# Optimization experiments

Measured on AMD Instinct MI355X. Metric: run time of the kernel, lower is better.

## Reference

```python
import jax, jax.numpy as jnp
import numpy as np
import math
from jax import lax

BATCH, SEQ_LEN, ENC_IN = 8, 2048, 1
D_MODEL, N_HEADS, E_LAYERS, D_FF, FACTOR, C_OUT = 512, 8, 3, 512, 5, 2
EPS = 1e-5


def _layernorm(x, g, b):
    mu = x.mean(-1, keepdims=True)
    var = ((x - mu) ** 2).mean(-1, keepdims=True)
    return (x - mu) / jnp.sqrt(var + EPS) * g + b


def _prob_attention(q, k, v, key):
    # q,k,v: [B,H,L,Dh]; ProbSparse: sample U keys per query, pick top-u queries by M = max - mean
    B, H, L, Dh = q.shape
    U = min(FACTOR * int(np.ceil(np.log(L))), L)  # U_part == u since L_Q == L_K
    idx = jax.random.randint(key, (L, U), 0, L)   # sampled key indices per query
    k_samp = k[:, :, idx, :]                       # [B,H,L,U,Dh]
    qk = jnp.einsum('bhld,bhlud->bhlu', q, k_samp)
    M = qk.max(-1) - qk.mean(-1)                   # sparsity measure [B,H,L]
    _, top = lax.top_k(M, U)                       # active query indices [B,H,U]
    q_red = jnp.take_along_axis(q, top[..., None], axis=2)
    scores = jnp.einsum('bhud,bhkd->bhuk', q_red, k) * (1.0 / math.sqrt(Dh))
    A = jax.nn.softmax(scores, axis=-1)
    ctx = jnp.broadcast_to(v.mean(axis=2, keepdims=True), q.shape)  # lazy-query context = mean(V)
    upd = jnp.einsum('bhuk,bhkd->bhud', A, v)
    b = jnp.arange(B)[:, None, None]
    h = jnp.arange(H)[None, :, None]
    return ctx.at[b, h, top].set(upd)


def _encoder_layer(x, p, key):
    Wq, Wk, Wv, bq, bk, bv, Wo, bo, W1, b1, W2, b2, g1, be1, g2, be2 = p
    B, L, dm = x.shape
    Dh = dm // N_HEADS
    split = lambda t: t.reshape(B, L, N_HEADS, Dh).transpose(0, 2, 1, 3)
    q = split(x @ Wq.T + bq)
    k = split(x @ Wk.T + bk)
    v = split(x @ Wv.T + bv)
    o = _prob_attention(q, k, v, key).transpose(0, 2, 1, 3).reshape(B, L, dm)
    x = _layernorm(x + o @ Wo.T + bo, g1, be1)
    y = jax.nn.gelu(x @ W1.T + b1, approximate=False) @ W2.T + b2  # 1x1 convs == linears
    return _layernorm(x + y, g2, be2)


def _distil_conv(x, w, b, g, be):
    # Conv1d(dm,dm,3, circular pad) -> BatchNorm(eval) -> ELU -> MaxPool1d(3, stride 2, pad 1)
    xc = jnp.pad(x.transpose(0, 2, 1), ((0, 0), (0, 0), (1, 1)), mode='wrap')
    y = lax.conv_general_dilated(xc, w, (1,), 'VALID', dimension_numbers=('NCH', 'OIH', 'NCH'))
    y = y + b[None, :, None]
    y = y / np.float32(np.sqrt(1.0 + EPS)) * g[None, :, None] + be[None, :, None]
    y = jax.nn.elu(y)
    y = lax.reduce_window(y, -jnp.inf, lax.max, (1, 1, 3), (1, 1, 2), [(0, 0), (0, 0), (1, 1)])
    return y.transpose(0, 2, 1)


def _forward(x_enc, tok_w, Wq, Wk, Wv, bq, bk, bv, Wo, bo, W1, b1, W2, b2,
             ln1_g, ln1_b, ln2_g, ln2_b, dc_w, dc_b, bn_g, bn_b, lnf_g, lnf_b, proj_w, proj_b):
    B, L = x_enc.shape
    dm = D_MODEL
    # TokenEmbedding: circular Conv1d(1, d_model, 3, bias=False)
    xc = jnp.pad(x_enc[:, None, :], ((0, 0), (0, 0), (1, 1)), mode='wrap')
    tok = lax.conv_general_dilated(xc, tok_w, (1,), 'VALID', dimension_numbers=('NCH', 'OIH', 'NCH'))
    tok = tok.transpose(0, 2, 1)  # [B,L,dm]
    # fixed sinusoidal positional embedding
    pos = jnp.arange(L, dtype=jnp.float32)[:, None]
    div = jnp.exp(jnp.arange(0, dm, 2, dtype=jnp.float32) * (-math.log(10000.0) / dm))
    pe = jnp.zeros((L, dm), jnp.float32).at[:, 0::2].set(jnp.sin(pos * div)).at[:, 1::2].set(jnp.cos(pos * div))
    x = tok + pe[None]
    key = jax.random.key(42)
    for i in range(E_LAYERS):
        p = (Wq[i], Wk[i], Wv[i], bq[i], bk[i], bv[i], Wo[i], bo[i],
             W1[i], b1[i], W2[i], b2[i], ln1_g[i], ln1_b[i], ln2_g[i], ln2_b[i])
        x = _encoder_layer(x, p, jax.random.fold_in(key, i))
        if i < E_LAYERS - 1:
            x = _distil_conv(x, dc_w[i], dc_b[i], bn_g[i], bn_b[i])
    x = _layernorm(x, lnf_g, lnf_b)
    return x.max(axis=1) @ proj_w.T + proj_b  # [B, C_OUT]


def setup_inputs() -> dict:
    key = jax.random.key(0)
    ks = jax.random.split(key, 12)
    dm, dff, L = D_MODEL, D_FF, E_LAYERS
    w = lambda k, shape, fan: jax.random.normal(k, shape, jnp.float32) / np.float32(np.sqrt(fan))
    return {
        'x_enc': jax.random.normal(ks[0], (BATCH, SEQ_LEN), jnp.float32),
        'tok_w': w(ks[1], (dm, ENC_IN, 3), 3 * ENC_IN),
        'Wq': w(ks[2], (L, dm, dm), dm), 'Wk': w(ks[3], (L, dm, dm), dm),
        'Wv': w(ks[4], (L, dm, dm), dm), 'Wo': w(ks[5], (L, dm, dm), dm),
        'bq': jnp.zeros((L, dm)), 'bk': jnp.zeros((L, dm)),
        'bv': jnp.zeros((L, dm)), 'bo': jnp.zeros((L, dm)),
        'W1': w(ks[6], (L, dff, dm), dm), 'b1': jnp.zeros((L, dff)),
        'W2': w(ks[7], (L, dm, dff), dff), 'b2': jnp.zeros((L, dm)),
        'ln1_g': jnp.ones((L, dm)), 'ln1_b': jnp.zeros((L, dm)),
        'ln2_g': jnp.ones((L, dm)), 'ln2_b': jnp.zeros((L, dm)),
        'dc_w': w(ks[8], (L - 1, dm, dm, 3), 3 * dm), 'dc_b': jnp.zeros((L - 1, dm)),
        'bn_g': jnp.ones((L - 1, dm)), 'bn_b': jnp.zeros((L - 1, dm)),
        'lnf_g': jnp.ones((dm,)), 'lnf_b': jnp.zeros((dm,)),
        'proj_w': w(ks[9], (C_OUT, dm), dm), 'proj_b': jnp.zeros((C_OUT,)),
    }


def reference(x_enc, tok_w, Wq, Wk, Wv, bq, bk, bv, Wo, bo, W1, b1, W2, b2,
              ln1_g, ln1_b, ln2_g, ln2_b, dc_w, dc_b, bn_g, bn_b, lnf_g, lnf_b, proj_w, proj_b):
    return _forward(x_enc, tok_w, Wq, Wk, Wv, bq, bk, bv, Wo, bo, W1, b1, W2, b2,
                    ln1_g, ln1_b, ln2_g, ln2_b, dc_w, dc_b, bn_g, bn_b, lnf_g, lnf_b, proj_w, proj_b)
```

## Files before the change

### kernel.cpp

```cpp
#include <hip/hip_runtime.h>

#define B_ 8
#define H_ 8
#define DM 512
#define DH 64
#define LMAX 2048
#define COUT 2

typedef __attribute__((ext_vector_type(8))) short frag8;
typedef __attribute__((ext_vector_type(4))) float f32x4;

typedef __attribute__((address_space(1))) const unsigned int guint;
typedef __attribute__((address_space(3))) unsigned int luint;
__device__ __forceinline__ void dma16(const short* g, short* l) {
  __builtin_amdgcn_global_load_lds((guint*)g, (luint*)l, 16, 0, 0);
}

__device__ __forceinline__ short f2bf(float v) {
  unsigned u = __float_as_uint(v);
  unsigned r = (u + 0x7fffu + ((u >> 16) & 1u)) >> 16;
  return (short)r;
}
__device__ __forceinline__ float bf2f(short s) {
  return __uint_as_float(((unsigned)(unsigned short)s) << 16);
}

__device__ __forceinline__ void tf2x32(unsigned k0, unsigned k1, unsigned x0, unsigned x1,
                                       unsigned& o0, unsigned& o1) {
  unsigned ks2 = k0 ^ k1 ^ 0x1BD11BDAu;
  x0 += k0; x1 += k1;
#define RND(r) { x0 += x1; x1 = (x1 << r) | (x1 >> (32 - r)); x1 ^= x0; }
  RND(13) RND(15) RND(26) RND(6)  x0 += k1;  x1 += ks2 + 1u;
  RND(17) RND(29) RND(16) RND(24) x0 += ks2; x1 += k0 + 2u;
  RND(13) RND(15) RND(26) RND(6)  x0 += k0;  x1 += k1 + 3u;
  RND(17) RND(29) RND(16) RND(24) x0 += k1;  x1 += ks2 + 4u;
  RND(13) RND(15) RND(26) RND(6)  x0 += ks2; x1 += k0 + 5u;
#undef RND
  o0 = x0; o1 = x1;
}

__global__ void idx_kernel(int* __restrict__ idxArr, int L, int U, int layer) {
  int p = blockIdx.x * 256 + threadIdx.x;
  int half = L * U;
  if (p >= half) return;
  unsigned fk0, fk1, k20, k21, o0, o1;
  tf2x32(0u, 42u, 0u, (unsigned)layer, fk0, fk1);
  tf2x32(fk0, fk1, 0u, 1u, k20, k21);
  tf2x32(k20, k21, 0u, (unsigned)p, o0, o1);
  idxArr[p] = (int)((o0 ^ o1) & (unsigned)(L - 1));
}

__global__ void embed_kernel(const float* __restrict__ xe, const float* __restrict__ tw,
                             float* __restrict__ X) {
  int i = blockIdx.x * 256 + threadIdx.x;
  int c = i % DM;
  int l = (i / DM) % LMAX;
  int b = i / (DM * LMAX);
  int lm = (l + LMAX - 1) & (LMAX - 1);
  int lp = (l + 1) & (LMAX - 1);
  const float* xb = xe + b * LMAX;
  float tok = tw[c * 3 + 0] * xb[lm] + tw[c * 3 + 1] * xb[l] + tw[c * 3 + 2] * xb[lp];
  float freq = expf(-(float)(c & ~1) * (9.210340371976184f / 512.0f));
  float ang = (float)l * freq;
  float pe = (c & 1) ? cosf(ang) : sinf(ang);
  X[i] = tok + pe;
}

__global__ void wsplit_kernel(const float* __restrict__ W, short* __restrict__ P0,
                              short* __restrict__ P1, short* __restrict__ P2, int n) {
  int i = blockIdx.x * 256 + threadIdx.x;
  if (i >= n) return;
  float v = W[i];
  short h0 = f2bf(v);
  float r1 = v - bf2f(h0);
  short h1 = f2bf(r1);
  float r2 = r1 - bf2f(h1);
  P0[i] = h0; P1[i] = h1; P2[i] = f2bf(r2);
}

__global__ void wt3_kernel(const float* __restrict__ w, short* __restrict__ P0,
                           short* __restrict__ P1, short* __restrict__ P2) {
  int i = blockIdx.x * 256 + threadIdx.x;
  int n = i / 1536, r = i - n * 1536, tap = r >> 9, k = r & 511;
  float v = w[((size_t)n * DM + k) * 3 + tap];
  short h0 = f2bf(v);
  float r1 = v - bf2f(h0);
  short h1 = f2bf(r1);
  float r2 = r1 - bf2f(h1);
  P0[i] = h0; P1[i] = h1; P2[i] = f2bf(r2);
}

template <int ACT, int QKV, int ACC, int CONV>
__global__ __launch_bounds__(256) void mgemm(const short* __restrict__ A0g,
                                             const short* __restrict__ A1g,
                                             const short* __restrict__ A2g,
                                             const short* __restrict__ W0g,
                                             const short* __restrict__ W1g,
                                             const short* __restrict__ W2g,
                                             const float* __restrict__ bias,
                                             float* __restrict__ C, int L, int Ktot) {
  __shared__ short A0[128 * 32], A1[128 * 32], A2[128 * 32];
  __shared__ short B0[128 * 32], B1[128 * 32], B2[128 * 32];
  int tid = threadIdx.x;
  int lane = tid & 63, wave = tid >> 6;
  int crow = lane >> 2, ckq = lane & 3;
  int gx = gridDim.x;
  int flat = blockIdx.y * gx + blockIdx.x;
  int mB, nB;
  if ((gridDim.y & 7) == 0) {
    int phase = flat & 7, sup = flat >> 3;
    nB = sup % gx;
    mB = phase + 8 * (sup / gx);
  } else {
    nB = blockIdx.x; mB = blockIdx.y;
  }
  int n0 = nB * 128, m0 = mB * 128;
  int wm = (wave >> 1) * 64, wn = (wave & 1) * 64;
  f32x4 acc[4][4] = {};
  int lrow = lane & 15, lq = lane >> 4;

  for (int k0 = 0; k0 < Ktot; k0 += 32) {
    int tap = 0, kcol = k0;
    if (CONV) { tap = k0 >> 9; kcol = k0 & 511; }
#pragma unroll
    for (int q = 0; q < 6; ++q) {
      int gc = wave * 6 + q;
      int pl = gc >> 3, c = gc & 7;
      int grow = m0 + c * 16 + crow;
      const short* gp;
      if (CONV) {
        int b = grow / L, l = grow - b * L;
        int le = l + tap - 1;
        le = (le < 0) ? le + L : (le >= L ? le - L : le);
        gp = ((size_t)(b * L + le) * DM + kcol + ckq * 8) +
             (pl == 0 ? A0g : pl == 1 ? A1g : A2g);
      } else {
        gp = ((size_t)grow * DM + k0 + ckq * 8) +
             (pl == 0 ? A0g : pl == 1 ? A1g : A2g);
      }
      short* lp = (pl == 0 ? A0 : pl == 1 ? A1 : A2) + c * 512;
      dma16(gp, lp);
    }
#pragma unroll
    for (int q = 0; q < 6; ++q) {
      int gc = wave * 6 + q;
      int pl = gc >> 3, c = gc & 7;
      int grow = n0 + c * 16 + crow;
      const short* gp = ((size_t)grow * Ktot + k0 + ckq * 8) +
                        (pl == 0 ? W0g : pl == 1 ? W1g : W2g);
      short* lp = (pl == 0 ? B0 : pl == 1 ? B1 : B2) + c * 512;
      dma16(gp, lp);
    }
    __syncthreads();
    frag8 a0f[4], a1f[4], a2f[4];
#pragma unroll
    for (int ti = 0; ti < 4; ++ti) {
      int off = (wm + ti * 16 + lrow) * 32 + lq * 8;
      a0f[ti] = *(const frag8*)&A0[off];
      a1f[ti] = *(const frag8*)&A1[off];
      a2f[ti] = *(const frag8*)&A2[off];
    }
#pragma unroll
    for (int tj = 0; tj < 4; ++tj) {
      int off = (wn + tj * 16 + lrow) * 32 + lq * 8;
      frag8 b0 = *(const frag8*)&B0[off];
      frag8 b1 = *(const frag8*)&B1[off];
      frag8 b2 = *(const frag8*)&B2[off];
#pragma unroll
      for (int ti = 0; ti < 4; ++ti) {
        f32x4 ac = acc[ti][tj];
        ac = __builtin_amdgcn_mfma_f32_16x16x32_bf16(a1f[ti], b1, ac, 0, 0, 0);
        ac = __builtin_amdgcn_mfma_f32_16x16x32_bf16(a0f[ti], b2, ac, 0, 0, 0);
        ac = __builtin_amdgcn_mfma_f32_16x16x32_bf16(a2f[ti], b0, ac, 0, 0, 0);
        ac = __builtin_amdgcn_mfma_f32_16x16x32_bf16(a0f[ti], b1, ac, 0, 0, 0);
        ac = __builtin_amdgcn_mfma_f32_16x16x32_bf16(a1f[ti], b0, ac, 0, 0, 0);
        ac = __builtin_amdgcn_mfma_f32_16x16x32_bf16(a0f[ti], b0, ac, 0, 0, 0);
        acc[ti][tj] = ac;
      }
    }
    __syncthreads();
  }
#pragma unroll
  for (int ti = 0; ti < 4; ++ti) {
#pragma unroll
    for (int tj = 0; tj < 4; ++tj) {
#pragma unroll
      for (int r = 0; r < 4; ++r) {
        int row = m0 + wm + ti * 16 + lq * 4 + r;
        int col = n0 + wn + tj * 16 + lrow;
        float v = acc[ti][tj][r];
        if (!CONV) v += bias[col];
        if (ACT) v = 0.5f * v * (1.0f + erff(v * 0.70710678118654752f));
        if (QKV) {
          int b = row / L, l = row - b * L;
          int h = col >> 6, d = col & 63;
          C[(((size_t)b * H_ + h) * L + l) * DH + d] = v;
        } else if (ACC) {
          C[(size_t)row * DM + col] += v;
        } else {
          C[(size_t)row * DM + col] = v;
        }
      }
    }
  }
}

__global__ void bnelu_kernel(float* __restrict__ Y, const float* __restrict__ cb,
                             const float* __restrict__ g, const float* __restrict__ be) {
  int i = blockIdx.x * 256 + threadIdx.x;
  int c = i % DM;
  const float invs = 0.9999950000374997f;
  float z = Y[i] + cb[c];
  z = z * invs * g[c] + be[c];
  Y[i] = z > 0.f ? z : expm1f(z);
}

template <int U>
__global__ void qkM_t(const float* __restrict__ Q, const float* __restrict__ Kd,
                      const int* __restrict__ idxArr, float* __restrict__ Mout, int L) {
  int lane = threadIdx.x & 63, wv = threadIdx.x >> 6;
  int row = blockIdx.x * 4 + wv;
  int l = row % L, bh = row / L;
  int u = lane & 7, dc = lane >> 3;
  const float* Qb = Q + ((size_t)bh * L + l) * DH + dc * 8;
  float4 q0 = *(const float4*)(Qb);
  float4 q1 = *(const float4*)(Qb + 4);
  const float* Kb = Kd + (size_t)bh * L * DH;
  const int* ip = idxArr + l * U;
  const int NP = (U + 7) / 8;
  float mx = -1e30f, sm = 0.f;
#pragma unroll
  for (int p = 0; p < NP; ++p) {
    int s = p * 8 + u;
    bool valid = (s < U);
    int ki = ip[valid ? s : 0];
    const float* kr = Kb + (size_t)ki * DH + dc * 8;
    float4 k0 = *(const float4*)(kr);
    float4 k1 = *(const float4*)(kr + 4);
    float d = q0.x * k0.x + q0.y * k0.y + q0.z * k0.z + q0.w * k0.w +
              q1.x * k1.x + q1.y * k1.y + q1.z * k1.z + q1.w * k1.w;
    d += __shfl_xor(d, 8, 64);
    d += __shfl_xor(d, 16, 64);
    d += __shfl_xor(d, 32, 64);
    if (valid) { mx = fmaxf(mx, d); sm += d; }
  }
#pragma unroll
  for (int o = 1; o <= 4; o <<= 1) {
    mx = fmaxf(mx, __shfl_xor(mx, o, 64));
    sm += __shfl_xor(sm, o, 64);
  }
  if (lane == 0) Mout[row] = mx - sm / (float)U;
}

__global__ void topk_kernel(const float* __restrict__ M, int* __restrict__ top, int L, int U) {
  __shared__ float vals[LMAX];
  __shared__ float rv[256];
  __shared__ int ri[256];
  int bh = blockIdx.x, tid = threadIdx.x;
  for (int j = tid; j < L; j += 256) vals[j] = M[(size_t)bh * L + j];
  __syncthreads();
  for (int u = 0; u < U; ++u) {
    float bv = -1e30f; int bi = L;
    for (int j = tid; j < L; j += 256) {
      float v = vals[j];
      if (v > bv) { bv = v; bi = j; }
    }
    rv[tid] = bv; ri[tid] = bi;
    __syncthreads();
    for (int s = 128; s >= 1; s >>= 1) {
      if (tid < s) {
        float ov = rv[tid + s]; int oi = ri[tid + s];
        if (ov > rv[tid] || (ov == rv[tid] && oi < ri[tid])) { rv[tid] = ov; ri[tid] = oi; }
      }
      __syncthreads();
    }
    if (tid == 0) { top[bh * U + u] = ri[0]; vals[ri[0]] = -1e30f; }
    __syncthreads();
  }
}

__global__ void vmean_kernel(const float* __restrict__ V, float* __restrict__ VM, int L) {
  __shared__ float red[256];
  int bh = blockIdx.x, tid = threadIdx.x, d = tid & 63, sq = tid >> 6;
  float s = 0.f;
  for (int l = sq; l < L; l += 4) s += V[((size_t)bh * L + l) * DH + d];
  red[tid] = s;
  __syncthreads();
  if (sq == 0) VM[bh * DH + d] = (red[d] + red[d + 64] + red[d + 128] + red[d + 192]) / (float)L;
}

__global__ void fill_kernel(const float* __restrict__ VM, float* __restrict__ O, int L) {
  size_t i = (size_t)blockIdx.x * 256 + threadIdx.x;
  int c = (int)(i % DM);
  int b = (int)(i / ((size_t)L * DM));
  O[i] = VM[b * DM + c];
}

__global__ __launch_bounds__(256) void attn_fused(const float* __restrict__ Q,
                                                  const float* __restrict__ Kd,
                                                  const float* __restrict__ V,
                                                  const int* __restrict__ top,
                                                  float* __restrict__ O, int L, int U) {
  __shared__ float Qs[8][64];
  __shared__ float Kt[64][65];
  __shared__ float Vs[64][68];
  __shared__ float ps[8][64];
  __shared__ int lst[8];
  int nch = (U + 7) >> 3;
  int bh = blockIdx.x / nch, ch = blockIdx.x - bh * nch;
  int u0g = ch * 8;
  int qn = U - u0g; if (qn > 8) qn = 8;
  int tid = threadIdx.x, lane = tid & 63, wv = tid >> 6;
  if (tid < qn) lst[tid] = top[bh * U + u0g + tid];
  __syncthreads();
  for (int idx = tid; idx < qn * 64; idx += 256) {
    int u = idx >> 6, d = idx & 63;
    Qs[u][d] = Q[((size_t)bh * L + lst[u]) * DH + d];
  }
  __syncthreads();
  int ua = wv, ub = wv + 4;
  bool hasA = ua < qn, hasB = ub < qn;
  float m0 = -1e30f, l0 = 0.f, o0 = 0.f;
  float m1 = -1e30f, l1 = 0.f, o1 = 0.f;
  const float* Kbase = Kd + (size_t)bh * L * DH;
  const float* Vbase = V + (size_t)bh * L * DH;
  for (int t0 = 0; t0 < L; t0 += 64) {
#pragma unroll
    for (int it = 0; it < 4; ++it) {
      int idx = tid + it * 256;
      int j = idx >> 4, d4 = (idx & 15) * 4;
      float4 kv = *(const float4*)(Kbase + (size_t)(t0 + j) * DH + d4);
      Kt[d4 + 0][j] = kv.x; Kt[d4 + 1][j] = kv.y;
      Kt[d4 + 2][j] = kv.z; Kt[d4 + 3][j] = kv.w;
      *(float4*)&Vs[j][d4] = *(const float4*)(Vbase + (size_t)(t0 + j) * DH + d4);
    }
    __syncthreads();
    float s0 = 0.f, s1 = 0.f;
#pragma unroll 16
    for (int d = 0; d < 64; ++d) {
      float kd = Kt[d][lane];
      s0 += kd * Qs[ua & 7][d];
      s1 += kd * Qs[ub & 7][d];
    }
    s0 *= 0.125f; s1 *= 0.125f;
    if (hasA) {
      float tm = s0;
#pragma unroll
      for (int o = 32; o >= 1; o >>= 1) tm = fmaxf(tm, __shfl_xor(tm, o, 64));
      float nm = fmaxf(m0, tm);
      float alpha = expf(m0 - nm);
      float p = expf(s0 - nm);
      float tsum = p;
#pragma unroll
      for (int o = 32; o >= 1; o >>= 1) tsum += __shfl_xor(tsum, o, 64);
      l0 = l0 * alpha + tsum;
      m0 = nm;
      ps[ua][lane] = p;
      o0 *= alpha;
    }
    if (hasB) {
      float tm = s1;
#pragma unroll
      for (int o = 32; o >= 1; o >>= 1) tm = fmaxf(tm, __shfl_xor(tm, o, 64));
      float nm = fmaxf(m1, tm);
      float alpha = expf(m1 - nm);
      float p = expf(s1 - nm);
      float tsum = p;
#pragma unroll
      for (int o = 32; o >= 1; o >>= 1) tsum += __shfl_xor(tsum, o, 64);
      l1 = l1 * alpha + tsum;
      m1 = nm;
      ps[ub][lane] = p;
      o1 *= alpha;
    }
    if (hasA) {
#pragma unroll 16
      for (int j = 0; j < 64; ++j) o0 += ps[ua][j] * Vs[j][lane];
    }
    if (hasB) {
#pragma unroll 16
      for (int j = 0; j < 64; ++j) o1 += ps[ub][j] * Vs[j][lane];
    }
    __syncthreads();
  }
  int b = bh / H_, h = bh - b * H_;
  if (hasA) O[((size_t)b * L + lst[ua]) * DM + h * DH + lane] = o0 / l0;
  if (hasB) O[((size_t)b * L + lst[ub]) * DM + h * DH + lane] = o1 / l1;
}

__global__ void ln_kernel(float* __restrict__ X, const float* __restrict__ g,
                          const float* __restrict__ be) {
  __shared__ float red[256];
  int row = blockIdx.x, tid = threadIdx.x;
  size_t base = (size_t)row * DM;
  float t0 = X[base + tid];
  float t1 = X[base + tid + 256];
  red[tid] = t0 + t1;
  __syncthreads();
  for (int s = 128; s >= 1; s >>= 1) { if (tid < s) red[tid] += red[tid + s]; __syncthreads(); }
  float mu = red[0] / 512.0f;
  __syncthreads();
  float d0 = t0 - mu, d1 = t1 - mu;
  red[tid] = d0 * d0 + d1 * d1;
  __syncthreads();
  for (int s = 128; s >= 1; s >>= 1) { if (tid < s) red[tid] += red[tid + s]; __syncthreads(); }
  float rstd = 1.0f / sqrtf(red[0] / 512.0f + 1e-5f);
  X[base + tid] = d0 * rstd * g[tid] + be[tid];
  X[base + tid + 256] = d1 * rstd * g[tid + 256] + be[tid + 256];
}

__global__ void pool_kernel(const float* __restrict__ Y, float* __restrict__ X, int L2) {
  int i = blockIdx.x * 256 + threadIdx.x;
  int c = i % DM;
  int t = (i / DM) % L2;
  int b = i / (DM * L2);
  int L = L2 * 2;
  const float* yb = Y + (size_t)b * L * DM + c;
  float m = fmaxf(yb[(size_t)(2 * t) * DM], yb[(size_t)(2 * t + 1) * DM]);
  if (t > 0) m = fmaxf(m, yb[(size_t)(2 * t - 1) * DM]);
  X[i] = m;
}

__global__ void colmax1_kernel(const float* __restrict__ X, float* __restrict__ P, int L) {
  int nlc = L >> 6;
  int bl = blockIdx.x;
  int b = bl / nlc, lc = bl % nlc;
  const float* xb = X + ((size_t)b * L + lc * 64) * DM;
  for (int c = threadIdx.x; c < DM; c += 256) {
    float m = -1e30f;
    for (int r = 0; r < 64; ++r) m = fmaxf(m, xb[(size_t)r * DM + c]);
    P[((size_t)b * nlc + lc) * DM + c] = m;
  }
}
__global__ void colmax2_kernel(const float* __restrict__ P, float* __restrict__ mc, int nlc) {
  int i = blockIdx.x * 256 + threadIdx.x;
  int b = i / DM, c = i % DM;
  float m = -1e30f;
  for (int lc = 0; lc < nlc; ++lc) m = fmaxf(m, P[((size_t)b * nlc + lc) * DM + c]);
  mc[i] = m;
}

__global__ void proj_kernel(const float* __restrict__ mc, const float* __restrict__ pw,
                            const float* __restrict__ pb, float* __restrict__ out) {
  __shared__ float red[256];
  int bo = blockIdx.x, b = bo / COUT, o = bo % COUT, tid = threadIdx.x;
  float s = mc[b * DM + tid] * pw[o * DM + tid] +
            mc[b * DM + tid + 256] * pw[o * DM + tid + 256];
  red[tid] = s;
  __syncthreads();
  for (int st = 128; st >= 1; st >>= 1) { if (tid < st) red[tid] += red[tid + st]; __syncthreads(); }
  if (tid == 0) out[bo] = red[0] + pb[o];
}

extern "C" void kernel_launch(void* const* d_in, const int* in_sizes, int n_in,
                              void* d_out, int out_size, void* d_ws, size_t ws_size,
                              hipStream_t stream) {
  (void)in_sizes; (void)n_in; (void)out_size;
  const float* xe   = (const float*)d_in[0];
  const float* tw   = (const float*)d_in[1];
  const float* Wq   = (const float*)d_in[2];
  const float* Wk   = (const float*)d_in[3];
  const float* Wv   = (const float*)d_in[4];
  const float* Wo   = (const float*)d_in[5];
  const float* bq   = (const float*)d_in[6];
  const float* bk   = (const float*)d_in[7];
  const float* bv   = (const float*)d_in[8];
  const float* bo   = (const float*)d_in[9];
  const float* W1   = (const float*)d_in[10];
  const float* b1   = (const float*)d_in[11];
  const float* W2   = (const float*)d_in[12];
  const float* b2   = (const float*)d_in[13];
  const float* ln1g = (const float*)d_in[14];
  const float* ln1b = (const float*)d_in[15];
  const float* ln2g = (const float*)d_in[16];
  const float* ln2b = (const float*)d_in[17];
  const float* dcw  = (const float*)d_in[18];
  const float* dcb  = (const float*)d_in[19];
  const float* bng  = (const float*)d_in[20];
  const float* bnb  = (const float*)d_in[21];
  const float* lnfg = (const float*)d_in[22];
  const float* lnfb = (const float*)d_in[23];
  const float* pw   = (const float*)d_in[24];
  const float* pb   = (const float*)d_in[25];
  float* out = (float*)d_out;

  float* Wf = (float*)d_ws;
  const size_t NB  = (size_t)B_ * LMAX * DM;
  const size_t NHB = (size_t)H_ * LMAX * DH;
  const size_t S_IDX = 81920, S_MV = 131072, S_TOP = 4096, S_VM = 4096,
               S_MC = 4096, S_P = 32768;
  const size_t PLANE  = (size_t)512 * 1536;
  const size_t APLANE = NB;
  const size_t S_WP = 3 * PLANE / 2 + 1024;
  const size_t S_AP = 3 * APLANE / 2 + 1024;
  const size_t SMALL = S_IDX + S_MV + S_TOP + S_VM + S_MC + S_P + S_WP + S_AP + 1024;

  int g = 8;
  while (g > 1 && (2 * NB + 3 * (size_t)g * NHB + SMALL) * 4 > ws_size) g >>= 1;

  float* X  = Wf;
  float* T  = X + NB;
  float* Q  = T + NB;
  float* K  = Q + (size_t)g * NHB;
  float* V  = K + (size_t)g * NHB;
  float* SM = V + (size_t)g * NHB;
  int*   IDX = (int*)SM;
  float* Mv  = SM + S_IDX;
  int*   TOP = (int*)(Mv + S_MV);
  float* VM  = Mv + S_MV + S_TOP;
  float* MC  = VM + S_VM;
  float* P   = MC + S_MC;
  short* WP0 = (short*)(P + S_P);
  short* WP1 = WP0 + PLANE;
  short* WP2 = WP1 + PLANE;
  short* AP0 = (short*)((float*)(P + S_P) + S_WP);
  short* AP1 = AP0 + APLANE;
  short* AP2 = AP1 + APLANE;

  embed_kernel<<<B_ * LMAX * DM / 256, 256, 0, stream>>>(xe, tw, X);

  int L = LMAX;
  for (int i = 0; i < 3; ++i) {
    int U = (i == 0) ? 40 : 35;
    size_t wOff = (size_t)i * DM * DM;
    int ng = B_ / g;
    int nch = (U + 7) >> 3;
    const int NW = DM * DM;

    idx_kernel<<<(L * U + 255) / 256, 256, 0, stream>>>(IDX, L, U, i);

    for (int gb = 0; gb < ng; ++gb) {
      const float* Xg = X + (size_t)gb * g * L * DM;
      float* Tg = T + (size_t)gb * g * L * DM;
      int Mg = g * L * DM;
      dim3 gq(DM / 128, g * L / 128);
      wsplit_kernel<<<Mg / 256, 256, 0, stream>>>(Xg, AP0, AP1, AP2, Mg);
      wsplit_kernel<<<NW / 256, 256, 0, stream>>>(Wq + wOff, WP0, WP1, WP2, NW);
      mgemm<0, 1, 0, 0><<<gq, 256, 0, stream>>>(AP0, AP1, AP2, WP0, WP1, WP2,
                                                bq + i * DM, Q, L, DM);
      wsplit_kernel<<<NW / 256, 256, 0, stream>>>(Wk + wOff, WP0, WP1, WP2, NW);
      mgemm<0, 1, 0, 0><<<gq, 256, 0, stream>>>(AP0, AP1, AP2, WP0, WP1, WP2,
                                                bk + i * DM, K, L, DM);
      wsplit_kernel<<<NW / 256, 256, 0, stream>>>(Wv + wOff, WP0, WP1, WP2, NW);
      mgemm<0, 1, 0, 0><<<gq, 256, 0, stream>>>(AP0, AP1, AP2, WP0, WP1, WP2,
                                                bv + i * DM, V, L, DM);
      if (U == 40) qkM_t<40><<<g * H_ * L / 4, 256, 0, stream>>>(Q, K, IDX, Mv, L);
      else         qkM_t<35><<<g * H_ * L / 4, 256, 0, stream>>>(Q, K, IDX, Mv, L);
      topk_kernel<<<g * H_, 256, 0, stream>>>(Mv, TOP, L, U);
      vmean_kernel<<<g * H_, 256, 0, stream>>>(V, VM, L);
      fill_kernel<<<(unsigned)((size_t)g * L * DM / 256), 256, 0, stream>>>(VM, Tg, L);
      attn_fused<<<g * H_ * nch, 256, 0, stream>>>(Q, K, V, TOP, Tg, L, U);
    }

    int Mf = B_ * L * DM;
    dim3 gf(DM / 128, B_ * L / 128);
    wsplit_kernel<<<Mf / 256, 256, 0, stream>>>(T, AP0, AP1, AP2, Mf);
    wsplit_kernel<<<NW / 256, 256, 0, stream>>>(Wo + wOff, WP0, WP1, WP2, NW);
    mgemm<0, 0, 1, 0><<<gf, 256, 0, stream>>>(AP0, AP1, AP2, WP0, WP1, WP2,
                                              bo + i * DM, X, L, DM);
    ln_kernel<<<B_ * L, 256, 0, stream>>>(X, ln1g + i * DM, ln1b + i * DM);
    wsplit_kernel<<<Mf / 256, 256, 0, stream>>>(X, AP0, AP1, AP2, Mf);
    wsplit_kernel<<<NW / 256, 256, 0, stream>>>(W1 + wOff, WP0, WP1, WP2, NW);
    mgemm<1, 0, 0, 0><<<gf, 256, 0, stream>>>(AP0, AP1, AP2, WP0, WP1, WP2,
                                              b1 + i * DM, T, L, DM);
    wsplit_kernel<<<Mf / 256, 256, 0, stream>>>(T, AP0, AP1, AP2, Mf);
    wsplit_kernel<<<NW / 256, 256, 0, stream>>>(W2 + wOff, WP0, WP1, WP2, NW);
    mgemm<0, 0, 1, 0><<<gf, 256, 0, stream>>>(AP0, AP1, AP2, WP0, WP1, WP2,
                                              b2 + i * DM, X, L, DM);
    ln_kernel<<<B_ * L, 256, 0, stream>>>(X, ln2g + i * DM, ln2b + i * DM);

    if (i < 2) {
      wsplit_kernel<<<Mf / 256, 256, 0, stream>>>(X, AP0, AP1, AP2, Mf);
      wt3_kernel<<<DM * 1536 / 256, 256, 0, stream>>>(dcw + (size_t)i * DM * DM * 3,
                                                      WP0, WP1, WP2);
      mgemm<0, 0, 0, 1><<<gf, 256, 0, stream>>>(AP0, AP1, AP2, WP0, WP1, WP2,
                                                nullptr, T, L, 1536);
      bnelu_kernel<<<B_ * L * DM / 256, 256, 0, stream>>>(T, dcb + i * DM, bng + i * DM,
                                                          bnb + i * DM);
      L >>= 1;
      pool_kernel<<<B_ * L * DM / 256, 256, 0, stream>>>(T, X, L);
    }
  }

  ln_kernel<<<B_ * L, 256, 0, stream>>>(X, lnfg, lnfb);
  colmax1_kernel<<<B_ * (L >> 6), 256, 0, stream>>>(X, P, L);
  colmax2_kernel<<<B_ * DM / 256, 256, 0, stream>>>(P, MC, L >> 6);
  proj_kernel<<<B_ * COUT, 256, 0, stream>>>(MC, pw, pb, out);
}
```

Baseline: 2.403 ms.

## Fuse bf16 three-way activation split into producer kernels and widen attention query chunks

```diff
diff --git a/kernel.cpp b/kernel.cpp
--- a/kernel.cpp
+++ b/kernel.cpp
@@ -23,6 +23,13 @@
 }
 __device__ __forceinline__ float bf2f(short s) {
   return __uint_as_float(((unsigned)(unsigned short)s) << 16);
+}
+__device__ __forceinline__ void split3(float v, short* p0, short* p1, short* p2, size_t i) {
+  short h0 = f2bf(v);
+  float r1 = v - bf2f(h0);
+  short h1 = f2bf(r1);
+  float r2 = r1 - bf2f(h1);
+  p0[i] = h0; p1[i] = h1; p2[i] = f2bf(r2);
 }
 
 __device__ __forceinline__ void tf2x32(unsigned k0, unsigned k1, unsigned x0, unsigned x1,
@@ -51,7 +58,8 @@
 }
 
 __global__ void embed_kernel(const float* __restrict__ xe, const float* __restrict__ tw,
-                             float* __restrict__ X) {
+                             float* __restrict__ X, short* __restrict__ P0,
+                             short* __restrict__ P1, short* __restrict__ P2) {
   int i = blockIdx.x * 256 + threadIdx.x;
   int c = i % DM;
   int l = (i / DM) % LMAX;
@@ -63,19 +71,16 @@
   float freq = expf(-(float)(c & ~1) * (9.210340371976184f / 512.0f));
   float ang = (float)l * freq;
   float pe = (c & 1) ? cosf(ang) : sinf(ang);
-  X[i] = tok + pe;
+  float v = tok + pe;
+  X[i] = v;
+  split3(v, P0, P1, P2, (size_t)i);
 }
 
 __global__ void wsplit_kernel(const float* __restrict__ W, short* __restrict__ P0,
                               short* __restrict__ P1, short* __restrict__ P2, int n) {
   int i = blockIdx.x * 256 + threadIdx.x;
   if (i >= n) return;
-  float v = W[i];
-  short h0 = f2bf(v);
-  float r1 = v - bf2f(h0);
-  short h1 = f2bf(r1);
-  float r2 = r1 - bf2f(h1);
-  P0[i] = h0; P1[i] = h1; P2[i] = f2bf(r2);
+  split3(W[i], P0, P1, P2, (size_t)i);
 }
 
 __global__ void wt3_kernel(const float* __restrict__ w, short* __restrict__ P0,
@@ -83,11 +88,7 @@
   int i = blockIdx.x * 256 + threadIdx.x;
   int n = i / 1536, r = i - n * 1536, tap = r >> 9, k = r & 511;
   float v = w[((size_t)n * DM + k) * 3 + tap];
-  short h0 = f2bf(v);
-  float r1 = v - bf2f(h0);
-  short h1 = f2bf(r1);
-  float r2 = r1 - bf2f(h1);
-  P0[i] = h0; P1[i] = h1; P2[i] = f2bf(r2);
+  split3(v, P0, P1, P2, (size_t)i);
 }
 
 template <int ACT, int QKV, int ACC, int CONV>
@@ -289,27 +290,31 @@
   if (sq == 0) VM[bh * DH + d] = (red[d] + red[d + 64] + red[d + 128] + red[d + 192]) / (float)L;
 }
 
-__global__ void fill_kernel(const float* __restrict__ VM, float* __restrict__ O, int L) {
+__global__ void fill_kernel(const float* __restrict__ VM, short* __restrict__ P0,
+                            short* __restrict__ P1, short* __restrict__ P2, int L) {
   size_t i = (size_t)blockIdx.x * 256 + threadIdx.x;
   int c = (int)(i % DM);
   int b = (int)(i / ((size_t)L * DM));
-  O[i] = VM[b * DM + c];
+  split3(VM[b * DM + c], P0, P1, P2, i);
 }
 
 __global__ __launch_bounds__(256) void attn_fused(const float* __restrict__ Q,
                                                   const float* __restrict__ Kd,
                                                   const float* __restrict__ V,
                                                   const int* __restrict__ top,
-                                                  float* __restrict__ O, int L, int U) {
-  __shared__ float Qs[8][64];
+                                                  short* __restrict__ OP0,
+                                                  short* __restrict__ OP1,
+                                                  short* __restrict__ OP2,
+                                                  int L, int U) {
+  __shared__ float Qs[16][64];
   __shared__ float Kt[64][65];
   __shared__ float Vs[64][68];
   __shared__ float ps[8][64];
-  __shared__ int lst[8];
-  int nch = (U + 7) >> 3;
+  __shared__ int lst[16];
+  int nch = (U + 15) >> 4;
   int bh = blockIdx.x / nch, ch = blockIdx.x - bh * nch;
-  int u0g = ch * 8;
-  int qn = U - u0g; if (qn > 8) qn = 8;
+  int u0g = ch * 16;
+  int qn = U - u0g; if (qn > 16) qn = 16;
   int tid = threadIdx.x, lane = tid & 63, wv = tid >> 6;
   if (tid < qn) lst[tid] = top[bh * U + u0g + tid];
   __syncthreads();
@@ -319,9 +324,12 @@
   }
   __syncthreads();
   int ua = wv, ub = wv + 4;
-  bool hasA = ua < qn, hasB = ub < qn;
-  float m0 = -1e30f, l0 = 0.f, o0 = 0.f;
-  float m1 = -1e30f, l1 = 0.f, o1 = 0.f;
+  bool hA0 = (ua < qn), hB0 = (ub < qn);
+  bool hA1 = (8 + ua < qn), hB1 = (8 + ub < qn);
+  float m0a = -1e30f, l0a = 0.f, o0a = 0.f;
+  float m0b = -1e30f, l0b = 0.f, o0b = 0.f;
+  float m1a = -1e30f, l1a = 0.f, o1a = 0.f;
+  float m1b = -1e30f, l1b = 0.f, o1b = 0.f;
   const float* Kbase = Kd + (size_t)bh * L * DH;
   const float* Vbase = V + (size_t)bh * L * DH;
   for (int t0 = 0; t0 < L; t0 += 64) {
@@ -335,61 +343,82 @@
       *(float4*)&Vs[j][d4] = *(const float4*)(Vbase + (size_t)(t0 + j) * DH + d4);
     }
     __syncthreads();
-    float s0 = 0.f, s1 = 0.f;
-#pragma unroll 16
-    for (int d = 0; d < 64; ++d) {
-      float kd = Kt[d][lane];
-      s0 += kd * Qs[ua & 7][d];
-      s1 += kd * Qs[ub & 7][d];
-    }
-    s0 *= 0.125f; s1 *= 0.125f;
-    if (hasA) {
-      float tm = s0;
-#pragma unroll
-      for (int o = 32; o >= 1; o >>= 1) tm = fmaxf(tm, __shfl_xor(tm, o, 64));
-      float nm = fmaxf(m0, tm);
-      float alpha = expf(m0 - nm);
-      float p = expf(s0 - nm);
-      float tsum = p;
-#pragma unroll
-      for (int o = 32; o >= 1; o >>= 1) tsum += __shfl_xor(tsum, o, 64);
-      l0 = l0 * alpha + tsum;
-      m0 = nm;
-      ps[ua][lane] = p;
-      o0 *= alpha;
-    }
-    if (hasB) {
-      float tm = s1;
-#pragma unroll
-      for (int o = 32; o >= 1; o >>= 1) tm = fmaxf(tm, __shfl_xor(tm, o, 64));
-      float nm = fmaxf(m1, tm);
-      float alpha = expf(m1 - nm);
-      float p = expf(s1 - nm);
-      float tsum = p;
-#pragma unroll
-      for (int o = 32; o >= 1; o >>= 1) tsum += __shfl_xor(tsum, o, 64);
-      l1 = l1 * alpha + tsum;
-      m1 = nm;
-      ps[ub][lane] = p;
-      o1 *= alpha;
-    }
-    if (hasA) {
-#pragma unroll 16
-      for (int j = 0; j < 64; ++j) o0 += ps[ua][j] * Vs[j][lane];
-    }
-    if (hasB) {
-#pragma unroll 16
-      for (int j = 0; j < 64; ++j) o1 += ps[ub][j] * Vs[j][lane];
-    }
+#define SUBSTEP(QA, QB, mA, lA, oA, mB, lB, oB, HA, HB)                        \
+    {                                                                          \
+      float s0 = 0.f, s1 = 0.f;                                                \
+      _Pragma("unroll 16")                                                     \
+      for (int d = 0; d < 64; ++d) {                                           \
+        float kd = Kt[d][lane];                                                \
+        s0 += kd * Qs[QA][d];                                                  \
+        s1 += kd * Qs[QB][d];                                                  \
+      }                                                                        \
+      s0 *= 0.125f; s1 *= 0.125f;                                              \
+      if (HA) {                                                                \
+        float tm = s0;                                                         \
+        _Pragma("unroll")                                                      \
+        for (int o = 32; o >= 1; o >>= 1) tm = fmaxf(tm, __shfl_xor(tm, o, 64)); \
+        float nm = fmaxf(mA, tm);                                              \
+        float alpha = expf(mA - nm);                                           \
+        float p = expf(s0 - nm);                                               \
+        float tsum = p;                                                        \
+        _Pragma("unroll")                                                      \
+        for (int o = 32; o >= 1; o >>= 1) tsum += __shfl_xor(tsum, o, 64);     \
+        lA = lA * alpha + tsum;                                                \
+        mA = nm;                                                               \
+        ps[ua][lane] = p;                                                      \
+        oA *= alpha;                                                           \
+      }                                                                        \
+      if (HB) {                                                                \
+        float tm = s1;                                                         \
+        _Pragma("unroll")                                                      \
+        for (int o = 32; o >= 1; o >>= 1) tm = fmaxf(tm, __shfl_xor(tm, o, 64)); \
+        float nm = fmaxf(mB, tm);                                              \
+        float alpha = expf(mB - nm);                                           \
+        float p = expf(s1 - nm);                                               \
+        float tsum = p;                                                        \
+        _Pragma("unroll")                                                      \
+        for (int o = 32; o >= 1; o >>= 1) tsum += __shfl_xor(tsum, o, 64);     \
+        lB = lB * alpha + tsum;                                                \
+        mB = nm;                                                               \
+        ps[ub][lane] = p;                                                      \
+        oB *= alpha;                                                           \
+      }                                                                        \
+      if (HA) {                                                                \
+        _Pragma("unroll 16")                                                   \
+        for (int j = 0; j < 64; ++j) oA += ps[ua][j] * Vs[j][lane];            \
+      }                                                                        \
+      if (HB) {                                                                \
+        _Pragma("unroll 16")                                                   \
+        for (int j = 0; j < 64; ++j) oB += ps[ub][j] * Vs[j][lane];            \
+      }                                                                        \
+    }
+    SUBSTEP(ua, ub, m0a, l0a, o0a, m0b, l0b, o0b, hA0, hB0)
+    SUBSTEP(8 + ua, 8 + ub, m1a, l1a, o1a, m1b, l1b, o1b, hA1, hB1)
+#undef SUBSTEP
     __syncthreads();
   }
   int b = bh / H_, h = bh - b * H_;
-  if (hasA) O[((size_t)b * L + lst[ua]) * DM + h * DH + lane] = o0 / l0;
-  if (hasB) O[((size_t)b * L + lst[ub]) * DM + h * DH + lane] = o1 / l1;
+  if (hA0) {
+    size_t i = ((size_t)b * L + lst[ua]) * DM + h * DH + lane;
+    split3(o0a / l0a, OP0, OP1, OP2, i);
+  }
+  if (hB0) {
+    size_t i = ((size_t)b * L + lst[ub]) * DM + h * DH + lane;
+    split3(o0b / l0b, OP0, OP1, OP2, i);
+  }
+  if (hA1) {
+    size_t i = ((size_t)b * L + lst[8 + ua]) * DM + h * DH + lane;
+    split3(o1a / l1a, OP0, OP1, OP2, i);
+  }
+  if (hB1) {
+    size_t i = ((size_t)b * L + lst[8 + ub]) * DM + h * DH + lane;
+    split3(o1b / l1b, OP0, OP1, OP2, i);
+  }
 }
 
 __global__ void ln_kernel(float* __restrict__ X, const float* __restrict__ g,
-                          const float* __restrict__ be) {
+                          const float* __restrict__ be, short* __restrict__ P0,
+                          short* __restrict__ P1, short* __restrict__ P2) {
   __shared__ float red[256];
   int row = blockIdx.x, tid = threadIdx.x;
   size_t base = (size_t)row * DM;
@@ -405,11 +434,19 @@
   __syncthreads();
   for (int s = 128; s >= 1; s >>= 1) { if (tid < s) red[tid] += red[tid + s]; __syncthreads(); }
   float rstd = 1.0f / sqrtf(red[0] / 512.0f + 1e-5f);
-  X[base + tid] = d0 * rstd * g[tid] + be[tid];
-  X[base + tid + 256] = d1 * rstd * g[tid + 256] + be[tid + 256];
-}
-
-__global__ void pool_kernel(const float* __restrict__ Y, float* __restrict__ X, int L2) {
+  float v0 = d0 * rstd * g[tid] + be[tid];
+  float v1 = d1 * rstd * g[tid + 256] + be[tid + 256];
+  X[base + tid] = v0;
+  X[base + tid + 256] = v1;
+  if (P0) {
+    split3(v0, P0, P1, P2, base + tid);
+    split3(v1, P0, P1, P2, base + tid + 256);
+  }
+}
+
+__global__ void pool_kernel(const float* __restrict__ Y, float* __restrict__ X, int L2,
+                            short* __restrict__ P0, short* __restrict__ P1,
+                            short* __restrict__ P2) {
   int i = blockIdx.x * 256 + threadIdx.x;
   int c = i % DM;
   int t = (i / DM) % L2;
@@ -419,6 +456,7 @@
   float m = fmaxf(yb[(size_t)(2 * t) * DM], yb[(size_t)(2 * t + 1) * DM]);
   if (t > 0) m = fmaxf(m, yb[(size_t)(2 * t - 1) * DM]);
   X[i] = m;
+  split3(m, P0, P1, P2, (size_t)i);
 }
 
 __global__ void colmax1_kernel(const float* __restrict__ X, float* __restrict__ P, int L) {
@@ -517,49 +555,48 @@
   short* AP1 = AP0 + APLANE;
   short* AP2 = AP1 + APLANE;
 
-  embed_kernel<<<B_ * LMAX * DM / 256, 256, 0, stream>>>(xe, tw, X);
+  embed_kernel<<<B_ * LMAX * DM / 256, 256, 0, stream>>>(xe, tw, X, AP0, AP1, AP2);
 
   int L = LMAX;
   for (int i = 0; i < 3; ++i) {
     int U = (i == 0) ? 40 : 35;
     size_t wOff = (size_t)i * DM * DM;
     int ng = B_ / g;
-    int nch = (U + 7) >> 3;
+    int nch = (U + 15) >> 4;
     const int NW = DM * DM;
 
     idx_kernel<<<(L * U + 255) / 256, 256, 0, stream>>>(IDX, L, U, i);
 
     for (int gb = 0; gb < ng; ++gb) {
-      const float* Xg = X + (size_t)gb * g * L * DM;
-      float* Tg = T + (size_t)gb * g * L * DM;
+      size_t aoff = (size_t)gb * g * L * DM;
       int Mg = g * L * DM;
+      (void)Mg;
       dim3 gq(DM / 128, g * L / 128);
-      wsplit_kernel<<<Mg / 256, 256, 0, stream>>>(Xg, AP0, AP1, AP2, Mg);
       wsplit_kernel<<<NW / 256, 256, 0, stream>>>(Wq + wOff, WP0, WP1, WP2, NW);
-      mgemm<0, 1, 0, 0><<<gq, 256, 0, stream>>>(AP0, AP1, AP2, WP0, WP1, WP2,
-                                                bq + i * DM, Q, L, DM);
+      mgemm<0, 1, 0, 0><<<gq, 256, 0, stream>>>(AP0 + aoff, AP1 + aoff, AP2 + aoff,
+                                                WP0, WP1, WP2, bq + i * DM, Q, L, DM);
       wsplit_kernel<<<NW / 256, 256, 0, stream>>>(Wk + wOff, WP0, WP1, WP2, NW);
-      mgemm<0, 1, 0, 0><<<gq, 256, 0, stream>>>(AP0, AP1, AP2, WP0, WP1, WP2,
-                                                bk + i * DM, K, L, DM);
+      mgemm<0, 1, 0, 0><<<gq, 256, 0, stream>>>(AP0 + aoff, AP1 + aoff, AP2 + aoff,
+                                                WP0, WP1, WP2, bk + i * DM, K, L, DM);
       wsplit_kernel<<<NW / 256, 256, 0, stream>>>(Wv + wOff, WP0, WP1, WP2, NW);
-      mgemm<0, 1, 0, 0><<<gq, 256, 0, stream>>>(AP0, AP1, AP2, WP0, WP1, WP2,
-                                                bv + i * DM, V, L, DM);
+      mgemm<0, 1, 0, 0><<<gq, 256, 0, stream>>>(AP0 + aoff, AP1 + aoff, AP2 + aoff,
+                                                WP0, WP1, WP2, bv + i * DM, V, L, DM);
       if (U == 40) qkM_t<40><<<g * H_ * L / 4, 256, 0, stream>>>(Q, K, IDX, Mv, L);
       else         qkM_t<35><<<g * H_ * L / 4, 256, 0, stream>>>(Q, K, IDX, Mv, L);
       topk_kernel<<<g * H_, 256, 0, stream>>>(Mv, TOP, L, U);
       vmean_kernel<<<g * H_, 256, 0, stream>>>(V, VM, L);
-      fill_kernel<<<(unsigned)((size_t)g * L * DM / 256), 256, 0, stream>>>(VM, Tg, L);
-      attn_fused<<<g * H_ * nch, 256, 0, stream>>>(Q, K, V, TOP, Tg, L, U);
+      fill_kernel<<<(unsigned)((size_t)g * L * DM / 256), 256, 0, stream>>>(
+          VM, AP0 + aoff, AP1 + aoff, AP2 + aoff, L);
+      attn_fused<<<g * H_ * nch, 256, 0, stream>>>(Q, K, V, TOP, AP0 + aoff,
+                                                   AP1 + aoff, AP2 + aoff, L, U);
     }
 
     int Mf = B_ * L * DM;
     dim3 gf(DM / 128, B_ * L / 128);
-    wsplit_kernel<<<Mf / 256, 256, 0, stream>>>(T, AP0, AP1, AP2, Mf);
     wsplit_kernel<<<NW / 256, 256, 0, stream>>>(Wo + wOff, WP0, WP1, WP2, NW);
     mgemm<0, 0, 1, 0><<<gf, 256, 0, stream>>>(AP0, AP1, AP2, WP0, WP1, WP2,
                                               bo + i * DM, X, L, DM);
-    ln_kernel<<<B_ * L, 256, 0, stream>>>(X, ln1g + i * DM, ln1b + i * DM);
-    wsplit_kernel<<<Mf / 256, 256, 0, stream>>>(X, AP0, AP1, AP2, Mf);
+    ln_kernel<<<B_ * L, 256, 0, stream>>>(X, ln1g + i * DM, ln1b + i * DM, AP0, AP1, AP2);
     wsplit_kernel<<<NW / 256, 256, 0, stream>>>(W1 + wOff, WP0, WP1, WP2, NW);
     mgemm<1, 0, 0, 0><<<gf, 256, 0, stream>>>(AP0, AP1, AP2, WP0, WP1, WP2,
                                               b1 + i * DM, T, L, DM);
@@ -567,10 +604,8 @@
     wsplit_kernel<<<NW / 256, 256, 0, stream>>>(W2 + wOff, WP0, WP1, WP2, NW);
     mgemm<0, 0, 1, 0><<<gf, 256, 0, stream>>>(AP0, AP1, AP2, WP0, WP1, WP2,
                                               b2 + i * DM, X, L, DM);
-    ln_kernel<<<B_ * L, 256, 0, stream>>>(X, ln2g + i * DM, ln2b + i * DM);
-
     if (i < 2) {
-      wsplit_kernel<<<Mf / 256, 256, 0, stream>>>(X, AP0, AP1, AP2, Mf);
+      ln_kernel<<<B_ * L, 256, 0, stream>>>(X, ln2g + i * DM, ln2b + i * DM, AP0, AP1, AP2);
       wt3_kernel<<<DM * 1536 / 256, 256, 0, stream>>>(dcw + (size_t)i * DM * DM * 3,
                                                       WP0, WP1, WP2);
       mgemm<0, 0, 0, 1><<<gf, 256, 0, stream>>>(AP0, AP1, AP2, WP0, WP1, WP2,
@@ -578,11 +613,14 @@
       bnelu_kernel<<<B_ * L * DM / 256, 256, 0, stream>>>(T, dcb + i * DM, bng + i * DM,
                                                           bnb + i * DM);
       L >>= 1;
-      pool_kernel<<<B_ * L * DM / 256, 256, 0, stream>>>(T, X, L);
-    }
-  }
-
-  ln_kernel<<<B_ * L, 256, 0, stream>>>(X, lnfg, lnfb);
+      pool_kernel<<<B_ * L * DM / 256, 256, 0, stream>>>(T, X, L, AP0, AP1, AP2);
+    } else {
+      ln_kernel<<<B_ * L, 256, 0, stream>>>(X, ln2g + i * DM, ln2b + i * DM,
+                                            nullptr, nullptr, nullptr);
+    }
+  }
+
+  ln_kernel<<<B_ * L, 256, 0, stream>>>(X, lnfg, lnfb, nullptr, nullptr, nullptr);
   colmax1_kernel<<<B_ * (L >> 6), 256, 0, stream>>>(X, P, L);
   colmax2_kernel<<<B_ * DM / 256, 256, 0, stream>>>(P, MC, L >> 6);
   proj_kernel<<<B_ * COUT, 256, 0, stream>>>(MC, pw, pb, out);
```

Result: no change. 2.398 ms (-0.2%).
